# Kernel optimization log

Hardware: AMD Instinct MI355X
Metric: run time of the kernel (lower is better)

The kernel has to match this reference:

```python
import jax, jax.numpy as jnp
import numpy as np

B, T, IN, H, OUT = 4096, 28, 28, 1024, 10


def setup_inputs() -> dict:
    key = jax.random.key(0)
    ks = jax.random.split(key, 6)
    s_ih = 1.0 / np.sqrt(IN)
    s_h = 1.0 / np.sqrt(H)
    return {
        "x": jax.random.normal(ks[0], (B, T, IN), dtype=jnp.float32),
        "W_ih": jax.random.uniform(ks[1], (IN, 4 * H), jnp.float32, -s_ih, s_ih),
        "W_hh": jax.random.uniform(ks[2], (H, 4 * H), jnp.float32, -s_h, s_h),
        "b": jax.random.uniform(ks[3], (4 * H,), jnp.float32, -s_h, s_h),
        "Wc": jax.random.uniform(ks[4], (H, OUT), jnp.float32, -s_h, s_h),
        "bc": jax.random.uniform(ks[5], (OUT,), jnp.float32, -s_h, s_h),
    }


def _lstm_last_hidden(x, W_ih, W_hh, b):
    # Precompute input projections for all timesteps: [T, B, 4H]
    xg = jnp.einsum('bti,ig->tbg', x, W_ih) + b
    h0 = jnp.zeros((x.shape[0], W_hh.shape[0]), x.dtype)
    c0 = jnp.zeros_like(h0)

    def step(carry, xg_t):
        h, c = carry
        gates = xg_t + h @ W_hh  # [B, 4H]
        i, f, g, o = jnp.split(gates, 4, axis=-1)
        i = jax.nn.sigmoid(i)
        f = jax.nn.sigmoid(f)
        g = jnp.tanh(g)
        o = jax.nn.sigmoid(o)
        c = f * c + i * g
        h = o * jnp.tanh(c)
        return (h, c), None

    (h, _), _ = jax.lax.scan(step, (h0, c0), xg)
    return h


def reference(x, W_ih, W_hh, b, Wc, bc):
    h = _lstm_last_hidden(x, W_ih, W_hh, b)
    # dropout is identity at inference (eval mode)
    return h @ Wc + bc
```

## Files before the change

### kernel.cpp

```cpp
#include <hip/hip_runtime.h>
#include <stdint.h>

#define GLOBAL_AS __attribute__((address_space(1)))
#define LDS_AS    __attribute__((address_space(3)))

typedef __attribute__((ext_vector_type(8))) short  short8;
typedef __attribute__((ext_vector_type(4))) float  floatx4;

static constexpr int B_   = 4096;
static constexpr int T_   = 28;
static constexpr int IN_  = 28;
static constexpr int H_   = 1024;
static constexpr int G4_  = 4096;
static constexpr int OUT_ = 10;
static constexpr int NT_  = 16;

__device__ __forceinline__ float bf2f(unsigned short u) {
  union { uint32_t i; float f; } v; v.i = ((uint32_t)u) << 16; return v.f;
}
__device__ __forceinline__ unsigned short f2bf(float f) {
  union { float f; uint32_t i; } v; v.f = f;
  uint32_t x = v.i;
  uint32_t lsb = (x >> 16) & 1u;
  x += 0x7fffu + lsb;
  return (unsigned short)(x >> 16);
}
__device__ __forceinline__ float sigm(float x) {
  return __builtin_amdgcn_rcpf(1.f + __builtin_amdgcn_exp2f(-1.4426950408889634f * x));
}
__device__ __forceinline__ float tanh_f(float x) {
  return 1.f - 2.f * __builtin_amdgcn_rcpf(1.f + __builtin_amdgcn_exp2f(2.8853900817779268f * x));
}
__device__ __forceinline__ void stage16(const unsigned short* g, unsigned short* l) {
  __builtin_amdgcn_global_load_lds(
      (const GLOBAL_AS uint32_t*)g, (LDS_AS uint32_t*)l, 16, 0, 0);
}

__global__ __launch_bounds__(256) void conv_x_kernel(const float* __restrict__ x,
                                                     unsigned short* __restrict__ xb) {
  int row = blockIdx.x * 256 + threadIdx.x;
  int t  = row >> 12;
  int bb = row & 4095;
  const float* src = x + (bb * T_ + t) * IN_;
  unsigned short* dst = xb + row * 32;
#pragma unroll
  for (int k = 0; k < IN_; ++k) dst[k] = f2bf(src[k]);
  dst[28] = 0; dst[29] = 0; dst[30] = 0; dst[31] = 0;
}

__global__ __launch_bounds__(256) void perm_whh_kernel(const float* __restrict__ whh,
                                                       unsigned short* __restrict__ wp) {
  __shared__ float lds[64][17];
  int g64  = blockIdx.x >> 2;
  int gate = blockIdx.x & 3;
  int oc0  = gate * H_ + g64 * 16;
  int n0   = g64 * 64 + gate * 16;
  int tid  = threadIdx.x;
  for (int kc = 0; kc < 16; ++kc) {
    int k0 = kc * 64;
    __syncthreads();
#pragma unroll
    for (int e = 0; e < 4; ++e) {
      int idx = e * 256 + tid;
      int k = idx >> 4, cc = idx & 15;
      lds[k][cc] = whh[(k0 + k) * G4_ + oc0 + cc];
    }
    __syncthreads();
#pragma unroll
    for (int e = 0; e < 4; ++e) {
      int idx = e * 256 + tid;
      int n = idx >> 6, kk = idx & 63;
      wp[(n0 + n) * H_ + k0 + kk] = f2bf(lds[kk][n]);
    }
  }
}

__global__ __launch_bounds__(256) void perm_wih_kernel(const float* __restrict__ wih,
                                                       unsigned short* __restrict__ wip) {
  __shared__ float lds[28][17];
  int g64  = blockIdx.x >> 2;
  int gate = blockIdx.x & 3;
  int oc0  = gate * H_ + g64 * 16;
  int n0   = g64 * 64 + gate * 16;
  int tid  = threadIdx.x;
  for (int idx = tid; idx < 448; idx += 256) {
    int k = idx >> 4, cc = idx & 15;
    lds[k][cc] = wih[k * G4_ + oc0 + cc];
  }
  __syncthreads();
#pragma unroll
  for (int e = 0; e < 2; ++e) {
    int idx = e * 256 + tid;
    int n = idx >> 5, kk = idx & 31;
    wip[(n0 + n) * 32 + kk] = (kk < IN_) ? f2bf(lds[kk][n]) : (unsigned short)0;
  }
}

__global__ __launch_bounds__(512, 2) void lstm_step_kernel(
    const unsigned short* __restrict__ hprev,
    const unsigned short* __restrict__ wp,
    const unsigned short* __restrict__ xbt,
    const unsigned short* __restrict__ wip,
    const float* __restrict__ bias,
    float* __restrict__ cst,
    unsigned short* __restrict__ hnext,
    int first) {
  __shared__ __align__(16) unsigned short lds[65536];

  const int tid = threadIdx.x;
  const int w   = tid >> 6;
  const int l   = tid & 63;
  const int wm  = w >> 2;
  const int wn  = w & 3;
  const int lc  = l & 15;
  const int lk  = l >> 4;

  const int hid = blockIdx.x;
  const int lid = (hid & 7) * 32 + (hid >> 3);
  const int bx  = lid & 15, by = lid >> 4;
  const int m0  = bx * 256;
  const int n0  = by * 256;

  const int swz  = (lc & 7) << 4;
  const int swzx = (lc & 3) << 4;

  const int r8  = tid >> 3;
  const int c8  = (tid & 7) * 8;
  const int c8s = c8 ^ ((r8 & 7) * 8);
  const size_t aoff = (size_t)(m0 + r8) * H_ + c8s;
  const int bwn_low = r8 >> 5;
  const int bc31    = r8 & 31;
  const int rx   = tid >> 2;
  const int cx8  = (tid & 3) * 8;
  const int cx8s = cx8 ^ ((rx & 3) * 8);

  auto stageA = [&](int bufu, int kt, int i) {
    stage16(hprev + aoff + (size_t)i * (64 * H_) + kt * 64,
            lds + bufu + i * 4096 + tid * 8);
  };
  auto stageB = [&](int bufu, int kt, int j) {
    int col = n0 + (((j & 1) * 2 + bwn_low) * 64) + ((j >> 1) * 32) + bc31;
    stage16(wp + (size_t)col * H_ + c8s + kt * 64,
            lds + bufu + 16384 + j * 4096 + tid * 8);
  };
  auto stageXA = [&](int half) {
    int row = half * 128 + rx;
    stage16(xbt + (size_t)(m0 + row) * 32 + cx8s,
            lds + 32768 + half * 4096 + tid * 8);
  };
  auto stageXB = [&](int half) {
    int col = n0 + (rx >> 5) * 64 + half * 32 + (rx & 31);
    stage16(wip + (size_t)col * 32 + cx8s,
            lds + 32768 + 8192 + half * 4096 + tid * 8);
  };
  auto ldsr = [&](int byteoff) -> short8 {
    return *reinterpret_cast<const short8*>(reinterpret_cast<const char*>(lds) + byteoff);
  };

  floatx4 acc[8][4];
#pragma unroll
  for (int i = 0; i < 8; ++i)
#pragma unroll
    for (int j = 0; j < 4; ++j) acc[i][j] = (floatx4){0.f, 0.f, 0.f, 0.f};

  short8 a[4][2], b[2][2];

#define LOAD_A(PB, MH)                                                               \
  _Pragma("unroll") for (int m_ = 0; m_ < 4; ++m_)                                   \
  _Pragma("unroll") for (int k_ = 0; k_ < 2; ++k_)                                   \
    a[m_][k_] = ldsr((PB) + (wm * 128 + (MH) * 64 + m_ * 16 + lc) * 128 +            \
                     ((k_ * 64 + lk * 16) ^ swz));

#define LOAD_B(PB, NH)                                                               \
  _Pragma("unroll") for (int n_ = 0; n_ < 2; ++n_)                                   \
  _Pragma("unroll") for (int k_ = 0; k_ < 2; ++k_)                                   \
    b[n_][k_] = ldsr((PB) + 32768 + ((NH) * 128 + wn * 32 + n_ * 16 + lc) * 128 +    \
                     ((k_ * 64 + lk * 16) ^ swz));

#define MFMA_Q(MH, NH)                                                               \
  __builtin_amdgcn_s_setprio(1);                                                     \
  _Pragma("unroll") for (int m_ = 0; m_ < 4; ++m_)                                   \
  _Pragma("unroll") for (int n_ = 0; n_ < 2; ++n_)                                   \
  _Pragma("unroll") for (int k_ = 0; k_ < 2; ++k_)                                   \
    acc[(MH) * 4 + m_][(NH) * 2 + n_] = __builtin_amdgcn_mfma_f32_16x16x32_bf16(     \
        a[m_][k_], b[n_][k_], acc[(MH) * 4 + m_][(NH) * 2 + n_], 0, 0, 0);           \
  __builtin_amdgcn_s_setprio(0);

#define PH_BAR                                                                       \
  __builtin_amdgcn_sched_barrier(0);                                                 \
  __builtin_amdgcn_s_barrier();                                                      \
  __builtin_amdgcn_sched_barrier(0);

#define TILE_BAR(VM)                                                                 \
  __builtin_amdgcn_sched_barrier(0);                                                 \
  asm volatile("s_waitcnt vmcnt(" #VM ")" ::: "memory");                             \
  __builtin_amdgcn_s_barrier();                                                      \
  __builtin_amdgcn_sched_barrier(0);

  if (first) {
    stageXA(0); stageXA(1); stageXB(0); stageXB(1);
    TILE_BAR(0)
    short8 xb4[4];
#pragma unroll
    for (int nf = 0; nf < 4; ++nf)
      xb4[nf] = ldsr(65536 + 16384 +
                     ((nf >> 1) * 128 + wn * 32 + (nf & 1) * 16 + lc) * 64 +
                     ((lk * 16) ^ swzx));
#pragma unroll
    for (int mf = 0; mf < 8; ++mf) {
      short8 xa = ldsr(65536 + (wm * 128 + mf * 16 + lc) * 64 + ((lk * 16) ^ swzx));
#pragma unroll
      for (int nf = 0; nf < 4; ++nf)
        acc[mf][nf] = __builtin_amdgcn_mfma_f32_16x16x32_bf16(xa, xb4[nf], acc[mf][nf], 0, 0, 0);
    }
  } else {
    stageXA(0); stageXA(1); stageXB(0); stageXB(1);
#pragma unroll
    for (int j = 0; j < 4; ++j) stageB(0, 0, j);
#pragma unroll
    for (int i = 0; i < 4; ++i) stageA(0, 0, i);
    TILE_BAR(8)
    {
      short8 xb4[4];
#pragma unroll
      for (int nf = 0; nf < 4; ++nf)
        xb4[nf] = ldsr(65536 + 16384 +
                       ((nf >> 1) * 128 + wn * 32 + (nf & 1) * 16 + lc) * 64 +
                       ((lk * 16) ^ swzx));
      __builtin_amdgcn_s_setprio(1);
#pragma unroll
      for (int mf = 0; mf < 8; ++mf) {
        short8 xa = ldsr(65536 + (wm * 128 + mf * 16 + lc) * 64 + ((lk * 16) ^ swzx));
#pragma unroll
        for (int nf = 0; nf < 4; ++nf)
          acc[mf][nf] = __builtin_amdgcn_mfma_f32_16x16x32_bf16(xa, xb4[nf], acc[mf][nf], 0, 0, 0);
      }
      __builtin_amdgcn_s_setprio(0);
    }
    PH_BAR
#pragma unroll
    for (int j = 0; j < 4; ++j) stageB(32768, 1, j);
#pragma unroll
    for (int i = 0; i < 4; ++i) stageA(32768, 1, i);
    TILE_BAR(8)

    for (int kt = 0; kt < NT_; ++kt) {
      const int pbB = (kt & 1) * 65536;
      const int pbu = (kt & 1) * 32768;
      const int qbu = ((kt + 1) & 1) * 32768;

      LOAD_B(pbB, 0)
      LOAD_A(pbB, 0)
      if (kt + 1 < NT_) { stageB(qbu, kt + 1, 0); stageB(qbu, kt + 1, 1); }
      MFMA_Q(0, 0)
      PH_BAR

      LOAD_B(pbB, 1)
      if (kt + 2 < NT_) { stageA(pbu, kt + 2, 0); stageA(pbu, kt + 2, 2); }
      MFMA_Q(0, 1)
      PH_BAR

      LOAD_A(pbB, 1)
      if (kt + 2 < NT_) { stageB(pbu, kt + 2, 2); stageB(pbu, kt + 2, 3); }
      MFMA_Q(1, 1)
      PH_BAR

      LOAD_B(pbB, 0)
      if (kt + 2 < NT_) { stageA(pbu, kt + 2, 1); stageA(pbu, kt + 2, 3); }
      MFMA_Q(1, 0)
      if (kt == NT_ - 2) { TILE_BAR(0) }
      else               { TILE_BAR(6) }
    }
  }

  const int jj  = (by * 4 + wn) * 16 + lc;
  const float bi  = bias[jj];
  const float bf_ = bias[H_ + jj];
  const float bg_ = bias[2 * H_ + jj];
  const float bo_ = bias[3 * H_ + jj];
#pragma unroll
  for (int mf = 0; mf < 8; ++mf) {
    const int rbase = m0 + wm * 128 + mf * 16 + lk * 4;
#pragma unroll
    for (int r = 0; r < 4; ++r) {
      const size_t idx = (size_t)(rbase + r) * H_ + jj;
      float ig = sigm(acc[mf][0][r] + bi);
      float fg = sigm(acc[mf][1][r] + bf_);
      float gg = tanh_f(acc[mf][2][r] + bg_);
      float og = sigm(acc[mf][3][r] + bo_);
      float cp = first ? 0.f : cst[idx];
      float cn = fg * cp + ig * gg;
      cst[idx] = cn;
      hnext[idx] = f2bf(og * tanh_f(cn));
    }
  }
#undef LOAD_A
#undef LOAD_B
#undef MFMA_Q
#undef PH_BAR
#undef TILE_BAR
}

__global__ __launch_bounds__(256) void cls_kernel(const unsigned short* __restrict__ h,
                                                  const float* __restrict__ wc,
                                                  const float* __restrict__ bc,
                                                  float* __restrict__ out) {
  int w = threadIdx.x >> 6, l = threadIdx.x & 63;
  int row = blockIdx.x * 4 + w;
  float acc[OUT_];
#pragma unroll
  for (int o = 0; o < OUT_; ++o) acc[o] = 0.f;
  const unsigned short* hr = h + row * H_;
  for (int k = l; k < H_; k += 64) {
    float hv = bf2f(hr[k]);
#pragma unroll
    for (int o = 0; o < OUT_; ++o) acc[o] += hv * wc[k * OUT_ + o];
  }
#pragma unroll
  for (int o = 0; o < OUT_; ++o) {
    float v = acc[o];
#pragma unroll
    for (int s = 32; s > 0; s >>= 1) v += __shfl_down(v, s, 64);
    if (l == 0) out[row * OUT_ + o] = v + bc[o];
  }
}

extern "C" void kernel_launch(void* const* d_in, const int* in_sizes, int n_in,
                              void* d_out, int out_size, void* d_ws, size_t ws_size,
                              hipStream_t stream) {
  const float* x    = (const float*)d_in[0];
  const float* wih  = (const float*)d_in[1];
  const float* whh  = (const float*)d_in[2];
  const float* bias = (const float*)d_in[3];
  const float* wc   = (const float*)d_in[4];
  const float* bc   = (const float*)d_in[5];
  float* out = (float*)d_out;

  char* ws = (char*)d_ws;
  unsigned short* wp  = (unsigned short*)(ws);
  unsigned short* wip = (unsigned short*)(ws + 8388608);
  unsigned short* xb  = (unsigned short*)(ws + 8650752);
  unsigned short* h0  = (unsigned short*)(ws + 15990784);
  unsigned short* h1  = (unsigned short*)(ws + 24379392);
  float*          cst = (float*)(ws + 32768000);

  hipLaunchKernelGGL(conv_x_kernel,  dim3(448), dim3(256), 0, stream, x, xb);
  hipLaunchKernelGGL(perm_whh_kernel, dim3(256), dim3(256), 0, stream, whh, wp);
  hipLaunchKernelGGL(perm_wih_kernel, dim3(256), dim3(256), 0, stream, wih, wip);

  unsigned short* hb[2] = {h0, h1};
  for (int t = 0; t < T_; ++t) {
    unsigned short* hn = hb[t & 1];
    unsigned short* hp = hb[(t & 1) ^ 1];
    hipLaunchKernelGGL(lstm_step_kernel, dim3(256), dim3(512), 0, stream,
                       hp, wp, xb + (size_t)t * (B_ * 32), wip, bias, cst, hn,
                       (t == 0) ? 1 : 0);
  }
  hipLaunchKernelGGL(cls_kernel, dim3(1024), dim3(256), 0, stream, hb[1], wc, bc, out);
}
```

Measured before the change: 1.119 ms.

## Replace four-phase interleaved pipeline with simple double-buffered tile loop

Drops the four-phase schedule in the recurrent GEMM. That schedule split each K tile into quadrants, separated them with three intra-tile barriers, staged two tiles ahead and reloaded B fragments twice per tile. Each iteration now issues all global-to-LDS staging for the next tile up front, loads every B fragment once, runs two half-tile MFMA groups and ends with a single full waitcnt barrier. The aim is to cut barrier count and redundant LDS reads. In exchange the prefetch distance shrinks to one tile, the full vmcnt(0) wait may expose memory latency, and holding twice as many B fragments in registers raises VGPR pressure.

```diff
diff --git a/kernel.cpp b/kernel.cpp
--- a/kernel.cpp
+++ b/kernel.cpp
@@ -163,7 +163,16 @@
 #pragma unroll
     for (int j = 0; j < 4; ++j) acc[i][j] = (floatx4){0.f, 0.f, 0.f, 0.f};
 
-  short8 a[4][2], b[2][2];
+  short8 a[4][2];
+  short8 b[4][2];
+
+#define LOAD_B_ALL(PB)                                                               \
+  _Pragma("unroll") for (int nh_ = 0; nh_ < 2; ++nh_)                                \
+  _Pragma("unroll") for (int n_ = 0; n_ < 2; ++n_)                                   \
+  _Pragma("unroll") for (int k_ = 0; k_ < 2; ++k_)                                   \
+    b[nh_ * 2 + n_][k_] =                                                            \
+        ldsr((PB) + 32768 + (nh_ * 128 + wn * 32 + n_ * 16 + lc) * 128 +             \
+             ((k_ * 64 + lk * 16) ^ swz));
 
 #define LOAD_A(PB, MH)                                                               \
   _Pragma("unroll") for (int m_ = 0; m_ < 4; ++m_)                                   \
@@ -171,25 +180,15 @@
     a[m_][k_] = ldsr((PB) + (wm * 128 + (MH) * 64 + m_ * 16 + lc) * 128 +            \
                      ((k_ * 64 + lk * 16) ^ swz));
 
-#define LOAD_B(PB, NH)                                                               \
+#define MFMA_HALF(MH)                                                                \
+  __builtin_amdgcn_s_setprio(1);                                                     \
+  _Pragma("unroll") for (int m_ = 0; m_ < 4; ++m_)                                   \
+  _Pragma("unroll") for (int nh_ = 0; nh_ < 2; ++nh_)                                \
   _Pragma("unroll") for (int n_ = 0; n_ < 2; ++n_)                                   \
   _Pragma("unroll") for (int k_ = 0; k_ < 2; ++k_)                                   \
-    b[n_][k_] = ldsr((PB) + 32768 + ((NH) * 128 + wn * 32 + n_ * 16 + lc) * 128 +    \
-                     ((k_ * 64 + lk * 16) ^ swz));
-
-#define MFMA_Q(MH, NH)                                                               \
-  __builtin_amdgcn_s_setprio(1);                                                     \
-  _Pragma("unroll") for (int m_ = 0; m_ < 4; ++m_)                                   \
-  _Pragma("unroll") for (int n_ = 0; n_ < 2; ++n_)                                   \
-  _Pragma("unroll") for (int k_ = 0; k_ < 2; ++k_)                                   \
-    acc[(MH) * 4 + m_][(NH) * 2 + n_] = __builtin_amdgcn_mfma_f32_16x16x32_bf16(     \
-        a[m_][k_], b[n_][k_], acc[(MH) * 4 + m_][(NH) * 2 + n_], 0, 0, 0);           \
+    acc[(MH) * 4 + m_][nh_ * 2 + n_] = __builtin_amdgcn_mfma_f32_16x16x32_bf16(      \
+        a[m_][k_], b[nh_ * 2 + n_][k_], acc[(MH) * 4 + m_][nh_ * 2 + n_], 0, 0, 0);  \
   __builtin_amdgcn_s_setprio(0);
-
-#define PH_BAR                                                                       \
-  __builtin_amdgcn_sched_barrier(0);                                                 \
-  __builtin_amdgcn_s_barrier();                                                      \
-  __builtin_amdgcn_sched_barrier(0);
 
 #define TILE_BAR(VM)                                                                 \
   __builtin_amdgcn_sched_barrier(0);                                                 \
@@ -237,39 +236,24 @@
       }
       __builtin_amdgcn_s_setprio(0);
     }
-    PH_BAR
-#pragma unroll
-    for (int j = 0; j < 4; ++j) stageB(32768, 1, j);
-#pragma unroll
-    for (int i = 0; i < 4; ++i) stageA(32768, 1, i);
-    TILE_BAR(8)
+    TILE_BAR(0)
 
     for (int kt = 0; kt < NT_; ++kt) {
       const int pbB = (kt & 1) * 65536;
-      const int pbu = (kt & 1) * 32768;
       const int qbu = ((kt + 1) & 1) * 32768;
 
-      LOAD_B(pbB, 0)
+      if (kt + 1 < NT_) {
+#pragma unroll
+        for (int j = 0; j < 4; ++j) stageB(qbu, kt + 1, j);
+#pragma unroll
+        for (int i = 0; i < 4; ++i) stageA(qbu, kt + 1, i);
+      }
+      LOAD_B_ALL(pbB)
       LOAD_A(pbB, 0)
-      if (kt + 1 < NT_) { stageB(qbu, kt + 1, 0); stageB(qbu, kt + 1, 1); }
-      MFMA_Q(0, 0)
-      PH_BAR
-
-      LOAD_B(pbB, 1)
-      if (kt + 2 < NT_) { stageA(pbu, kt + 2, 0); stageA(pbu, kt + 2, 2); }
-      MFMA_Q(0, 1)
-      PH_BAR
-
+      MFMA_HALF(0)
       LOAD_A(pbB, 1)
-      if (kt + 2 < NT_) { stageB(pbu, kt + 2, 2); stageB(pbu, kt + 2, 3); }
-      MFMA_Q(1, 1)
-      PH_BAR
-
-      LOAD_B(pbB, 0)
-      if (kt + 2 < NT_) { stageA(pbu, kt + 2, 1); stageA(pbu, kt + 2, 3); }
-      MFMA_Q(1, 0)
-      if (kt == NT_ - 2) { TILE_BAR(0) }
-      else               { TILE_BAR(6) }
+      MFMA_HALF(1)
+      if (kt + 1 < NT_) { TILE_BAR(0) }
     }
   }
 
@@ -294,10 +278,9 @@
       hnext[idx] = f2bf(og * tanh_f(cn));
     }
   }
+#undef LOAD_B_ALL
 #undef LOAD_A
-#undef LOAD_B
-#undef MFMA_Q
-#undef PH_BAR
+#undef MFMA_HALF
 #undef TILE_BAR
 }
 
```

Result: no change. 1.127 ms (+0.7%).

## Unroll K loop by two with double-buffered B fragments and split barriers

Applied to the files above, without the earlier changes.

Restructures the recurrent GEMM main loop to process two K tiles per iteration, ping-ponging B register fragments (bA/bB) so the next B fragment is loaded from LDS while the current quadrant's MFMAs run. Each phase now uses a barrier plus an explicit lgkmcnt wait before the MFMAs and a second barrier after them. The goal is to hide LDS read latency behind matrix math and keep global staging overlapped. The cost is roughly twice as many barriers per tile and higher register pressure, which could offset the gains.

```diff
diff --git a/kernel.cpp b/kernel.cpp
--- a/kernel.cpp
+++ b/kernel.cpp
@@ -163,43 +163,50 @@
 #pragma unroll
     for (int j = 0; j < 4; ++j) acc[i][j] = (floatx4){0.f, 0.f, 0.f, 0.f};
 
-  short8 a[4][2], b[2][2];
-
-#define LOAD_A(PB, MH)                                                               \
+  short8 a[4][2], bA[2][2], bB[2][2];
+
+#define LOAD_A_TO(ARR, PB, MH)                                                       \
   _Pragma("unroll") for (int m_ = 0; m_ < 4; ++m_)                                   \
   _Pragma("unroll") for (int k_ = 0; k_ < 2; ++k_)                                   \
-    a[m_][k_] = ldsr((PB) + (wm * 128 + (MH) * 64 + m_ * 16 + lc) * 128 +            \
-                     ((k_ * 64 + lk * 16) ^ swz));
-
-#define LOAD_B(PB, NH)                                                               \
+    ARR[m_][k_] = ldsr((PB) + (wm * 128 + (MH) * 64 + m_ * 16 + lc) * 128 +          \
+                       ((k_ * 64 + lk * 16) ^ swz));
+
+#define LOAD_B_TO(ARR, PB, NH)                                                       \
   _Pragma("unroll") for (int n_ = 0; n_ < 2; ++n_)                                   \
   _Pragma("unroll") for (int k_ = 0; k_ < 2; ++k_)                                   \
-    b[n_][k_] = ldsr((PB) + 32768 + ((NH) * 128 + wn * 32 + n_ * 16 + lc) * 128 +    \
-                     ((k_ * 64 + lk * 16) ^ swz));
-
-#define MFMA_Q(MH, NH)                                                               \
+    ARR[n_][k_] = ldsr((PB) + 32768 + ((NH) * 128 + wn * 32 + n_ * 16 + lc) * 128 +  \
+                       ((k_ * 64 + lk * 16) ^ swz));
+
+#define MFMA_Q(AR, BR, MH, NH)                                                       \
   __builtin_amdgcn_s_setprio(1);                                                     \
   _Pragma("unroll") for (int m_ = 0; m_ < 4; ++m_)                                   \
   _Pragma("unroll") for (int n_ = 0; n_ < 2; ++n_)                                   \
   _Pragma("unroll") for (int k_ = 0; k_ < 2; ++k_)                                   \
     acc[(MH) * 4 + m_][(NH) * 2 + n_] = __builtin_amdgcn_mfma_f32_16x16x32_bf16(     \
-        a[m_][k_], b[n_][k_], acc[(MH) * 4 + m_][(NH) * 2 + n_], 0, 0, 0);           \
+        AR[m_][k_], BR[n_][k_], acc[(MH) * 4 + m_][(NH) * 2 + n_], 0, 0, 0);         \
   __builtin_amdgcn_s_setprio(0);
 
-#define PH_BAR                                                                       \
+#define SYNC_MID                                                                     \
+  __builtin_amdgcn_sched_barrier(0);                                                 \
+  __builtin_amdgcn_s_barrier();                                                      \
+  asm volatile("s_waitcnt lgkmcnt(0)" ::: "memory");                                 \
+  __builtin_amdgcn_sched_barrier(0);
+
+#define SYNC_MID_V(VM)                                                               \
+  __builtin_amdgcn_sched_barrier(0);                                                 \
+  asm volatile("s_waitcnt vmcnt(" #VM ")" ::: "memory");                             \
+  __builtin_amdgcn_s_barrier();                                                      \
+  asm volatile("s_waitcnt lgkmcnt(0)" ::: "memory");                                 \
+  __builtin_amdgcn_sched_barrier(0);
+
+#define SYNC_END                                                                     \
   __builtin_amdgcn_sched_barrier(0);                                                 \
   __builtin_amdgcn_s_barrier();                                                      \
   __builtin_amdgcn_sched_barrier(0);
 
-#define TILE_BAR(VM)                                                                 \
-  __builtin_amdgcn_sched_barrier(0);                                                 \
-  asm volatile("s_waitcnt vmcnt(" #VM ")" ::: "memory");                             \
-  __builtin_amdgcn_s_barrier();                                                      \
-  __builtin_amdgcn_sched_barrier(0);
-
   if (first) {
     stageXA(0); stageXA(1); stageXB(0); stageXB(1);
-    TILE_BAR(0)
+    SYNC_MID_V(0)
     short8 xb4[4];
 #pragma unroll
     for (int nf = 0; nf < 4; ++nf)
@@ -219,7 +226,7 @@
     for (int j = 0; j < 4; ++j) stageB(0, 0, j);
 #pragma unroll
     for (int i = 0; i < 4; ++i) stageA(0, 0, i);
-    TILE_BAR(8)
+    SYNC_MID_V(8)
     {
       short8 xb4[4];
 #pragma unroll
@@ -236,40 +243,61 @@
           acc[mf][nf] = __builtin_amdgcn_mfma_f32_16x16x32_bf16(xa, xb4[nf], acc[mf][nf], 0, 0, 0);
       }
       __builtin_amdgcn_s_setprio(0);
-    }
-    PH_BAR
+      asm volatile("s_waitcnt lgkmcnt(0)" ::: "memory");
+      __builtin_amdgcn_sched_barrier(0);
+    }
+    SYNC_END
 #pragma unroll
     for (int j = 0; j < 4; ++j) stageB(32768, 1, j);
 #pragma unroll
     for (int i = 0; i < 4; ++i) stageA(32768, 1, i);
-    TILE_BAR(8)
-
-    for (int kt = 0; kt < NT_; ++kt) {
-      const int pbB = (kt & 1) * 65536;
-      const int pbu = (kt & 1) * 32768;
-      const int qbu = ((kt + 1) & 1) * 32768;
-
-      LOAD_B(pbB, 0)
-      LOAD_A(pbB, 0)
-      if (kt + 1 < NT_) { stageB(qbu, kt + 1, 0); stageB(qbu, kt + 1, 1); }
-      MFMA_Q(0, 0)
-      PH_BAR
-
-      LOAD_B(pbB, 1)
-      if (kt + 2 < NT_) { stageA(pbu, kt + 2, 0); stageA(pbu, kt + 2, 2); }
-      MFMA_Q(0, 1)
-      PH_BAR
-
-      LOAD_A(pbB, 1)
-      if (kt + 2 < NT_) { stageB(pbu, kt + 2, 2); stageB(pbu, kt + 2, 3); }
-      MFMA_Q(1, 1)
-      PH_BAR
-
-      LOAD_B(pbB, 0)
-      if (kt + 2 < NT_) { stageA(pbu, kt + 2, 1); stageA(pbu, kt + 2, 3); }
-      MFMA_Q(1, 0)
-      if (kt == NT_ - 2) { TILE_BAR(0) }
-      else               { TILE_BAR(6) }
+    SYNC_MID_V(0)
+    LOAD_B_TO(bA, 0, 0)
+    asm volatile("s_waitcnt lgkmcnt(0)" ::: "memory");
+    __builtin_amdgcn_sched_barrier(0);
+    SYNC_END
+
+    for (int kt = 0; kt < NT_; kt += 2) {
+      LOAD_A_TO(a, 0, 0)
+      if (kt + 2 < NT_) { stageB(0, kt + 2, 0); stageB(0, kt + 2, 1); }
+      SYNC_MID
+      MFMA_Q(a, bA, 0, 0)
+      SYNC_END
+      LOAD_B_TO(bB, 0, 1)
+      if (kt + 2 < NT_) { stageA(0, kt + 2, 0); stageA(0, kt + 2, 2); }
+      SYNC_MID
+      MFMA_Q(a, bB, 0, 1)
+      SYNC_END
+      LOAD_A_TO(a, 0, 1)
+      if (kt + 2 < NT_) { stageB(0, kt + 2, 2); stageB(0, kt + 2, 3); }
+      SYNC_MID
+      MFMA_Q(a, bB, 1, 1)
+      SYNC_END
+      LOAD_B_TO(bB, 65536, 0)
+      if (kt + 2 < NT_) { stageA(0, kt + 2, 1); stageA(0, kt + 2, 3); }
+      if (kt == NT_ - 2) { SYNC_MID_V(0) } else { SYNC_MID_V(6) }
+      MFMA_Q(a, bA, 1, 0)
+      SYNC_END
+      LOAD_A_TO(a, 65536, 0)
+      if (kt + 3 < NT_) { stageB(32768, kt + 3, 0); stageB(32768, kt + 3, 1); }
+      SYNC_MID
+      MFMA_Q(a, bB, 0, 0)
+      SYNC_END
+      LOAD_B_TO(bA, 65536, 1)
+      if (kt + 3 < NT_) { stageA(32768, kt + 3, 0); stageA(32768, kt + 3, 2); }
+      SYNC_MID
+      MFMA_Q(a, bA, 0, 1)
+      SYNC_END
+      LOAD_A_TO(a, 65536, 1)
+      if (kt + 3 < NT_) { stageB(32768, kt + 3, 2); stageB(32768, kt + 3, 3); }
+      SYNC_MID
+      MFMA_Q(a, bA, 1, 1)
+      SYNC_END
+      LOAD_B_TO(bA, 0, 0)
+      if (kt + 3 < NT_) { stageA(32768, kt + 3, 1); stageA(32768, kt + 3, 3); }
+      SYNC_MID_V(6)
+      MFMA_Q(a, bB, 1, 0)
+      SYNC_END
     }
   }
 
@@ -294,11 +322,12 @@
       hnext[idx] = f2bf(og * tanh_f(cn));
     }
   }
-#undef LOAD_A
-#undef LOAD_B
+#undef LOAD_A_TO
+#undef LOAD_B_TO
 #undef MFMA_Q
-#undef PH_BAR
-#undef TILE_BAR
+#undef SYNC_MID
+#undef SYNC_MID_V
+#undef SYNC_END
 }
 
 __global__ __launch_bounds__(256) void cls_kernel(const unsigned short* __restrict__ h,
```

Result: slower. 1.152 ms (+3.0%).
